# Kernel tuning notes

Measured on AMD Instinct MI355X. Metric: run time of the kernel, lower is better.

The kernel has to match this reference:

```python
import jax, jax.numpy as jnp
import numpy as np

N = 50000   # nodes
E = 800000  # edges (before self-loops)
IN = 128    # input feature dim
H = 4       # attention heads


def setup_inputs() -> dict:
    key = jax.random.key(0)
    ks = jax.random.split(key, 32)
    f = lambda k, s: (jax.random.normal(k, s, dtype=jnp.float32) * 0.1)
    inp = {
        "x": jax.random.normal(ks[0], (N, IN), dtype=jnp.float32),
        "edge_index": jax.random.randint(ks[1], (2, E), 0, N, dtype=jnp.int32),
        "edge_attr": jax.random.normal(ks[2], (E, 1), dtype=jnp.float32),
        # GATConv 1: 128 -> 8 per head, 4 heads (concat -> 32)
        "W1": f(ks[3], (IN, 32)), "as1": f(ks[4], (H, 8)), "ad1": f(ks[5], (H, 8)), "b1": jnp.zeros((32,), jnp.float32),
        # GATConv 2: 32 -> 16 per head (concat -> 64)
        "W2": f(ks[6], (32, 64)), "as2": f(ks[7], (H, 16)), "ad2": f(ks[8], (H, 16)), "b2": jnp.zeros((64,), jnp.float32),
        # GATConv 3: 64 -> 32 per head (concat -> 128)
        "W3": f(ks[9], (64, 128)), "as3": f(ks[10], (H, 32)), "ad3": f(ks[11], (H, 32)), "b3": jnp.zeros((128,), jnp.float32),
        # GATConv 4: 128 -> 64 per head (concat -> 256)
        "W4": f(ks[12], (128, 256)), "as4": f(ks[13], (H, 64)), "ad4": f(ks[14], (H, 64)), "b4": jnp.zeros((256,), jnp.float32),
        # MLP head
        "Wr": f(ks[15], (256, 32)), "br": jnp.zeros((32,), jnp.float32),
        "Wf1": f(ks[16], (32, 64)), "bf1": jnp.zeros((64,), jnp.float32),
        "Wf2": f(ks[17], (64, 1)), "bf2": jnp.zeros((1,), jnp.float32),
    }
    return inp


def _gat_layer(x, W, a_src, a_dst, bias, src, dst):
    """PyG GATConv (concat=True, negative_slope=0.2, self-loops appended upstream)."""
    heads, C = a_src.shape
    h = (x @ W).reshape(-1, heads, C)              # [N, H, C]
    alpha_s = jnp.sum(h * a_src[None], axis=-1)    # [N, H]
    alpha_d = jnp.sum(h * a_dst[None], axis=-1)    # [N, H]
    e = jax.nn.leaky_relu(alpha_s[src] + alpha_d[dst], 0.2)  # [E', H]
    # segment softmax over incoming edges of each destination node
    emax = jax.ops.segment_max(e, dst, num_segments=N)
    ee = jnp.exp(e - emax[dst])
    denom = jax.ops.segment_sum(ee, dst, num_segments=N)
    alpha = ee / denom[dst]                        # [E', H]
    msg = h[src] * alpha[:, :, None]               # [E', H, C]
    out = jax.ops.segment_sum(msg, dst, num_segments=N)  # [N, H, C]
    return out.reshape(-1, heads * C) + bias


def reference(x, edge_index, edge_attr,
              W1, as1, ad1, b1, W2, as2, ad2, b2,
              W3, as3, ad3, b3, W4, as4, ad4, b4,
              Wr, br, Wf1, bf1, Wf2, bf2):
    # edge_attr is accepted but unused, matching the original forward.
    loop = jnp.arange(N, dtype=edge_index.dtype)
    src = jnp.concatenate([edge_index[0], loop])   # add self-loops (PyG default)
    dst = jnp.concatenate([edge_index[1], loop])
    h = jax.nn.elu(_gat_layer(x, W1, as1, ad1, b1, src, dst))
    h = jax.nn.elu(_gat_layer(h, W2, as2, ad2, b2, src, dst))
    h = jax.nn.elu(_gat_layer(h, W3, as3, ad3, b3, src, dst))
    h = jax.nn.elu(_gat_layer(h, W4, as4, ad4, b4, src, dst))
    h = jax.nn.elu(h @ Wr + br)
    h = jax.nn.elu(h @ Wf1 + bf1)
    return h @ Wf2 + bf2                           # [N, 1]
```

## Files before the change

kernel.cpp:

```cpp
#include <hip/hip_runtime.h>
#include <hip/hip_fp16.h>
#include <math.h>

constexpr int NN = 50000;
constexpr int NE = 800000;
constexpr int NEP = NE + NN;
constexpr int CAP = 96;
constexpr int SCAT_B = (NEP + 255) / 256;
constexpr int PACK_B = 26;
constexpr int NT = (NN + 63) / 64;

typedef _Float16 half8_t __attribute__((ext_vector_type(8)));
typedef float    f32x4_t __attribute__((ext_vector_type(4)));

__device__ __forceinline__ float lrelu02(float x) { return x > 0.f ? x : 0.2f * x; }
__device__ __forceinline__ float eluf(float x)    { return x > 0.f ? x : (__expf(x) - 1.f); }
__device__ __forceinline__ float pick4(float4 q, int hd) {
  return (hd == 0) ? q.x : (hd == 1) ? q.y : (hd == 2) ? q.z : q.w;
}


__device__ __forceinline__ void pack_w_one(const float* __restrict__ W,
                                           __half* __restrict__ Wp,
                                           int M, int tid, int total) {
  if (tid >= total) return;
  int CT = M >> 4;
  int l = tid & 63;
  int c = (tid >> 6) % CT;
  int kc = (tid >> 6) / CT;
  int n = l & 15, q = l >> 4;
  __half* dst = Wp + (size_t)tid * 8;
  const float* src = W + (size_t)(kc * 32 + q * 8) * M + c * 16 + n;
  #pragma unroll
  for (int j = 0; j < 8; j++) dst[j] = __float2half_rn(src[j * M]);
}


template<int M, int C, int CT>
__device__ __forceinline__ void alpha_epilogue(const f32x4_t* acc,
    const float* __restrict__ a_src, const float* __restrict__ a_dst,
    int row_base, int m, float* __restrict__ as_out, float* __restrict__ ad_out) {
  float aS[CT], aD[CT];
  #pragma unroll
  for (int c = 0; c < CT; c++) { aS[c] = a_src[c * 16 + m]; aD[c] = a_dst[c * 16 + m]; }

  if constexpr (C == 8) {
    #pragma unroll
    for (int r = 0; r < 4; r++) {
      float p0 = acc[0][r] * aS[0], p1 = acc[1][r] * aS[1];
      float q0 = acc[0][r] * aD[0], q1 = acc[1][r] * aD[1];
      #pragma unroll
      for (int off = 1; off < 8; off <<= 1) {
        p0 += __shfl_xor(p0, off); p1 += __shfl_xor(p1, off);
        q0 += __shfl_xor(q0, off); q1 += __shfl_xor(q1, off);
      }
      int row = row_base + r;
      if ((m & 7) == 0 && row < NN) {
        int hb = m >> 3;
        as_out[row * 4 + hb]     = p0;
        as_out[row * 4 + 2 + hb] = p1;
        ad_out[row * 4 + hb]     = q0;
        ad_out[row * 4 + 2 + hb] = q1;
      }
    }
  } else {
    constexpr int FPH = C / 16;
    #pragma unroll
    for (int r = 0; r < 4; r++) {
      float bs[4] = {0.f, 0.f, 0.f, 0.f}, bd[4] = {0.f, 0.f, 0.f, 0.f};
      #pragma unroll
      for (int c = 0; c < CT; c++) {
        int hd = c / FPH;
        bs[hd] += acc[c][r] * aS[c];
        bd[hd] += acc[c][r] * aD[c];
      }
      #pragma unroll
      for (int off = 1; off < 16; off <<= 1)
        #pragma unroll
        for (int h = 0; h < 4; h++) {
          bs[h] += __shfl_xor(bs[h], off);
          bd[h] += __shfl_xor(bd[h], off);
        }
      int row = row_base + r;
      if (m < 4 && row < NN) {
        float vs = (m == 0) ? bs[0] : (m == 1) ? bs[1] : (m == 2) ? bs[2] : bs[3];
        float vd = (m == 0) ? bd[0] : (m == 1) ? bd[1] : (m == 2) ? bd[2] : bd[3];
        as_out[row * 4 + m] = vs;
        ad_out[row * 4 + m] = vd;
      }
    }
  }
}


__global__ __launch_bounds__(256) void front_kernel(
    const int* __restrict__ edge_src, const int* __restrict__ edge_dst,
    int* __restrict__ count, int* __restrict__ csr_src,
    const float* __restrict__ W1,
    const float* __restrict__ W2, __half* __restrict__ Wp2,
    const float* __restrict__ W3, __half* __restrict__ Wp3,
    const float* __restrict__ W4, __half* __restrict__ Wp4,
    const float* __restrict__ Wr, __half* __restrict__ Wrp,
    const float* __restrict__ Wf1, __half* __restrict__ Wf1p,
    const float* __restrict__ x, __half* __restrict__ Ch,
    const float* __restrict__ a_src, const float* __restrict__ a_dst,
    float* __restrict__ as_out, float* __restrict__ ad_out) {
  int b = blockIdx.x;
  if (b < SCAT_B) {
    int i = b * 256 + threadIdx.x;
    if (i < NEP) {
      int s, d;
      if (i < NE) { s = edge_src[i]; d = edge_dst[i]; } else { s = i - NE; d = s; }
      int pos = atomicAdd(&count[d], 1);
      if (pos < CAP) csr_src[d * CAP + pos] = s;
    }
    return;
  }
  if (b < SCAT_B + PACK_B) {
    int tid = (b - SCAT_B) * 256 + threadIdx.x;
    if (tid < 256)            pack_w_one(W2, Wp2, 64,  tid,        256);
    else if (tid < 1280)      pack_w_one(W3, Wp3, 128, tid - 256,  1024);
    else if (tid < 5376)      pack_w_one(W4, Wp4, 256, tid - 1280, 4096);
    else if (tid < 6400)      pack_w_one(Wr, Wrp, 32,  tid - 5376, 1024);
    else if (tid < 6656)      pack_w_one(Wf1, Wf1p, 64, tid - 6400, 256);
    return;
  }

  constexpr int M = 32, K = 128, CT = 2, KC = 4;
  __shared__ _Float16 Ah[64 * 40];
  __shared__ _Float16 Bs[KC * CT * 64 * 8];
  int t = threadIdx.x;
  int w = t >> 6, l = t & 63;
  int m = l & 15, q = l >> 4;
  int row0 = (b - SCAT_B - PACK_B) * 64;

  #pragma unroll
  for (int u0 = 0; u0 < 2; u0++) {
    int u = t + u0 * 256;
    int ul = u & 63;
    int uc = (u >> 6) & 1;
    int ukc = u >> 7;
    int un = ul & 15, uq = ul >> 4;
    const float* src = W1 + (size_t)(ukc * 32 + uq * 8) * M + uc * 16 + un;
    _Float16* dst = &Bs[u * 8];
    #pragma unroll
    for (int j = 0; j < 8; j++) dst[j] = (_Float16)src[j * M];
  }

  f32x4_t acc[CT];
  #pragma unroll
  for (int c = 0; c < CT; c++) acc[c] = (f32x4_t){0.f, 0.f, 0.f, 0.f};

  for (int kc = 0; kc < KC; kc++) {
    __syncthreads();
    #pragma unroll
    for (int i = 0; i < 2; i++) {
      int idx = t + 256 * i;
      int row = idx >> 3, c4 = idx & 7;
      int gr = row0 + row; if (gr >= NN) gr = NN - 1;
      float4 v = *(const float4*)(x + (size_t)gr * K + kc * 32 + c4 * 4);
      _Float16 h4[4] = {(_Float16)v.x, (_Float16)v.y, (_Float16)v.z, (_Float16)v.w};
      *(uint2*)(&Ah[row * 40 + c4 * 4]) = *(const uint2*)h4;
    }
    __syncthreads();
    half8_t a = *(const half8_t*)(&Ah[(w * 16 + m) * 40 + q * 8]);
    #pragma unroll
    for (int c = 0; c < CT; c++) {
      half8_t bf = *(const half8_t*)(&Bs[((kc * CT + c) * 64 + l) * 8]);
      acc[c] = __builtin_amdgcn_mfma_f32_16x16x32_f16(a, bf, acc[c], 0, 0, 0);
    }
  }

  #pragma unroll
  for (int r = 0; r < 4; r++) {
    int row = row0 + w * 16 + q * 4 + r;
    if (row < NN) {
      #pragma unroll
      for (int c = 0; c < CT; c++)
        Ch[(size_t)row * M + c * 16 + m] = __float2half_rn(acc[c][r]);
    }
  }
  alpha_epilogue<M, 8, CT>(acc, a_src, a_dst, row0 + w * 16 + q * 4, m, as_out, ad_out);
}


template<int M, int K, int C>
__global__ __launch_bounds__(256) void gemm_mfma_f16_kernel(const __half* __restrict__ A,
    const __half* __restrict__ Wp, __half* __restrict__ Ch,
    const float* __restrict__ a_src, const float* __restrict__ a_dst,
    float* __restrict__ as_out, float* __restrict__ ad_out) {
  constexpr int CT = M / 16;
  constexpr int KC = K / 32;
  __shared__ _Float16 Ah[64 * 40];
  int t = threadIdx.x;
  int w = t >> 6, l = t & 63;
  int m = l & 15, q = l >> 4;
  int row0 = blockIdx.x * 64;

  f32x4_t acc[CT];
  #pragma unroll
  for (int c = 0; c < CT; c++) acc[c] = (f32x4_t){0.f, 0.f, 0.f, 0.f};

  const half8_t* Bfrag = (const half8_t*)Wp;

  for (int kc = 0; kc < KC; kc++) {
    __syncthreads();
    {
      int row = t >> 2, c8 = t & 3;
      int gr = row0 + row; if (gr >= NN) gr = NN - 1;
      uint4 v = *(const uint4*)(A + (size_t)gr * K + kc * 32 + c8 * 8);
      *(uint4*)(&Ah[row * 40 + c8 * 8]) = v;
    }
    __syncthreads();
    half8_t a = *(const half8_t*)(&Ah[(w * 16 + m) * 40 + q * 8]);
    #pragma unroll
    for (int c = 0; c < CT; c++) {
      half8_t b = Bfrag[(kc * CT + c) * 64 + l];
      acc[c] = __builtin_amdgcn_mfma_f32_16x16x32_f16(a, b, acc[c], 0, 0, 0);
    }
  }

  #pragma unroll
  for (int r = 0; r < 4; r++) {
    int row = row0 + w * 16 + q * 4 + r;
    if (row < NN) {
      #pragma unroll
      for (int c = 0; c < CT; c++)
        Ch[(size_t)row * M + c * 16 + m] = __float2half_rn(acc[c][r]);
    }
  }
  alpha_epilogue<M, C, CT>(acc, a_src, a_dst, row0 + w * 16 + q * 4, m, as_out, ad_out);
}


template<int HC, int C>
__global__ __launch_bounds__(256) void agg_kernel(const __half* __restrict__ h,
    const float* __restrict__ as_v, const float* __restrict__ ad_v,
    const int* __restrict__ count, const int* __restrict__ csr_src,
    const float* __restrict__ bias, __half* __restrict__ out) {
  constexpr int V = HC / 8;
  constexpr int G = 64 / V;
  constexpr int P = 4;
  __shared__ float4 see4[4][CAP];
  __shared__ int    ssrc[4][CAP];
  int wid = threadIdx.x >> 6, lane = threadIdx.x & 63;
  int dst = blockIdx.x * 4 + wid;
  int base = dst * CAP;
  int deg = count[dst]; if (deg > CAP) deg = CAP;
  float4 ad = *(const float4*)(ad_v + dst * 4);

  float d0 = 0.f, d1 = 0.f, d2 = 0.f, d3 = 0.f;
  #pragma unroll
  for (int it = 0; it < 2; it++) {
    int j = lane + it * 64;
    if (j < deg) {
      int s = csr_src[base + j];
      float4 as = *(const float4*)(as_v + s * 4);
      float4 x = make_float4(__expf(lrelu02(as.x + ad.x)), __expf(lrelu02(as.y + ad.y)),
                             __expf(lrelu02(as.z + ad.z)), __expf(lrelu02(as.w + ad.w)));
      ssrc[wid][j] = s; see4[wid][j] = x;
      d0 += x.x; d1 += x.y; d2 += x.z; d3 += x.w;
    }
  }
  #pragma unroll
  for (int off = 32; off > 0; off >>= 1) {
    d0 += __shfl_xor(d0, off); d1 += __shfl_xor(d1, off);
    d2 += __shfl_xor(d2, off); d3 += __shfl_xor(d3, off);
  }
  float4 inv = make_float4(1.f / d0, 1.f / d1, 1.f / d2, 1.f / d3);

  int g = lane / V, v = lane % V;
  int hd = (v * 8) / C;
  float invh = pick4(inv, hd);
  int steps = (deg + G - 1) / G;
  const float4* hrows = (const float4*)h;

  float  px[P];
  float4 hv[P];
  #pragma unroll
  for (int k = 0; k < P; k++) {
    int jj = k * G + g;
    bool ok = jj < deg;
    int jc = ok ? jj : 0;
    int s = ssrc[wid][jc];
    float x = ((const float*)&see4[wid][jc])[hd];
    px[k] = ok ? x * invh : 0.f;
    hv[k] = hrows[(size_t)s * V + v];
  }

  float acc[8];
  #pragma unroll
  for (int i = 0; i < 8; i++) acc[i] = 0.f;
  int nB = (steps + P - 1) / P;
  for (int b = 1; b <= nB; b++) {
    #pragma unroll
    for (int k = 0; k < P; k++) {
      const __half2* hp = (const __half2*)&hv[k];
      float2 f0 = __half22float2(hp[0]);
      float2 f1 = __half22float2(hp[1]);
      float2 f2 = __half22float2(hp[2]);
      float2 f3 = __half22float2(hp[3]);
      float p = px[k];
      acc[0] += p * f0.x; acc[1] += p * f0.y;
      acc[2] += p * f1.x; acc[3] += p * f1.y;
      acc[4] += p * f2.x; acc[5] += p * f2.y;
      acc[6] += p * f3.x; acc[7] += p * f3.y;
      int jj = (b * P + k) * G + g;
      bool ok = jj < deg;
      int jc = ok ? jj : 0;
      int s = ssrc[wid][jc];
      float x = ((const float*)&see4[wid][jc])[hd];
      px[k] = ok ? x * invh : 0.f;
      hv[k] = hrows[(size_t)s * V + v];
    }
  }

  #pragma unroll
  for (int off = V; off < 64; off <<= 1)
    #pragma unroll
    for (int i = 0; i < 8; i++) acc[i] += __shfl_xor(acc[i], off);

  if (lane < V) {
    const float4* b4 = (const float4*)bias;
    float4 ba = b4[2 * v], bb = b4[2 * v + 1];
    _Float16 o[8];
    o[0] = (_Float16)eluf(acc[0] + ba.x); o[1] = (_Float16)eluf(acc[1] + ba.y);
    o[2] = (_Float16)eluf(acc[2] + ba.z); o[3] = (_Float16)eluf(acc[3] + ba.w);
    o[4] = (_Float16)eluf(acc[4] + bb.x); o[5] = (_Float16)eluf(acc[5] + bb.y);
    o[6] = (_Float16)eluf(acc[6] + bb.z); o[7] = (_Float16)eluf(acc[7] + bb.w);
    *(uint4*)(out + (size_t)dst * HC + v * 8) = *(const uint4*)o;
  }
}


__global__ __launch_bounds__(256) void mlp_mfma_kernel(const __half* __restrict__ h4,
    const __half* __restrict__ Wrp, const float* __restrict__ br,
    const __half* __restrict__ Wf1p, const float* __restrict__ bf1,
    const float* __restrict__ Wf2, const float* __restrict__ bf2,
    float* __restrict__ out) {
  __shared__ _Float16 rS[64 * 40];
  int t = threadIdx.x;
  int w = t >> 6, l = t & 63;
  int m = l & 15, q = l >> 4;
  int row0 = blockIdx.x * 64;
  const half8_t* Bwr  = (const half8_t*)Wrp;
  const half8_t* Bwf1 = (const half8_t*)Wf1p;

  int arow = row0 + w * 16 + m; if (arow >= NN) arow = NN - 1;
  const half8_t* Arow = (const half8_t*)(h4 + (size_t)arow * 256);
  half8_t afr[8];
  #pragma unroll
  for (int kc = 0; kc < 8; kc++) afr[kc] = Arow[kc * 4 + q];
  f32x4_t acc1[2];
  acc1[0] = (f32x4_t){0.f, 0.f, 0.f, 0.f};
  acc1[1] = (f32x4_t){0.f, 0.f, 0.f, 0.f};
  #pragma unroll
  for (int kc = 0; kc < 8; kc++) {
    acc1[0] = __builtin_amdgcn_mfma_f32_16x16x32_f16(afr[kc], Bwr[(kc * 2 + 0) * 64 + l], acc1[0], 0, 0, 0);
    acc1[1] = __builtin_amdgcn_mfma_f32_16x16x32_f16(afr[kc], Bwr[(kc * 2 + 1) * 64 + l], acc1[1], 0, 0, 0);
  }
  #pragma unroll
  for (int c = 0; c < 2; c++)
    #pragma unroll
    for (int r = 0; r < 4; r++) {
      float vv = eluf(acc1[c][r] + br[c * 16 + m]);
      rS[(w * 16 + q * 4 + r) * 40 + c * 16 + m] = (_Float16)vv;
    }
  __syncthreads();

  half8_t a2 = *(const half8_t*)(&rS[(w * 16 + m) * 40 + q * 8]);
  f32x4_t acc2[4];
  #pragma unroll
  for (int c = 0; c < 4; c++) acc2[c] = (f32x4_t){0.f, 0.f, 0.f, 0.f};
  #pragma unroll
  for (int c = 0; c < 4; c++)
    acc2[c] = __builtin_amdgcn_mfma_f32_16x16x32_f16(a2, Bwf1[c * 64 + l], acc2[c], 0, 0, 0);

  float wv[4] = {Wf2[m], Wf2[16 + m], Wf2[32 + m], Wf2[48 + m]};
  float rsum[4];
  #pragma unroll
  for (int r = 0; r < 4; r++) {
    float sr = 0.f;
    #pragma unroll
    for (int c = 0; c < 4; c++)
      sr += eluf(acc2[c][r] + bf1[c * 16 + m]) * wv[c];
    #pragma unroll
    for (int off = 1; off < 16; off <<= 1) sr += __shfl_xor(sr, off);
    rsum[r] = sr;
  }
  if (m == 0) {
    float b = bf2[0];
    #pragma unroll
    for (int r = 0; r < 4; r++) {
      int row = row0 + w * 16 + q * 4 + r;
      if (row < NN) out[row] = rsum[r] + b;
    }
  }
}


extern "C" void kernel_launch(void* const* d_in, const int* in_sizes, int n_in,
                              void* d_out, int out_size, void* d_ws, size_t ws_size,
                              hipStream_t stream) {
  const float* x   = (const float*)d_in[0];
  const int*   ei  = (const int*)d_in[1];
  const float* W1  = (const float*)d_in[3];
  const float* as1 = (const float*)d_in[4];
  const float* ad1 = (const float*)d_in[5];
  const float* b1  = (const float*)d_in[6];
  const float* W2  = (const float*)d_in[7];
  const float* as2 = (const float*)d_in[8];
  const float* ad2 = (const float*)d_in[9];
  const float* b2  = (const float*)d_in[10];
  const float* W3  = (const float*)d_in[11];
  const float* as3 = (const float*)d_in[12];
  const float* ad3 = (const float*)d_in[13];
  const float* b3  = (const float*)d_in[14];
  const float* W4  = (const float*)d_in[15];
  const float* as4 = (const float*)d_in[16];
  const float* ad4 = (const float*)d_in[17];
  const float* b4  = (const float*)d_in[18];
  const float* Wr  = (const float*)d_in[19];
  const float* br  = (const float*)d_in[20];
  const float* Wf1 = (const float*)d_in[21];
  const float* bf1 = (const float*)d_in[22];
  const float* Wf2 = (const float*)d_in[23];
  const float* bf2 = (const float*)d_in[24];
  float* out = (float*)d_out;

  char* p = (char*)d_ws;
  auto alloc = [&](size_t bytes) {
    char* q = p;
    p += (bytes + 255) & ~(size_t)255;
    return q;
  };
  int* count   = (int*)alloc((size_t)NN * 4);
  int* csr_src = (int*)alloc((size_t)NN * CAP * 4);
  __half* Hh = (__half*)alloc((size_t)NN * 256 * 2);
  __half* B2 = (__half*)alloc((size_t)NN * 128 * 2);
  __half* B3 = (__half*)alloc((size_t)NN * 256 * 2);
  float* as_buf = (float*)alloc((size_t)NN * 4 * 4);
  float* ad_buf = (float*)alloc((size_t)NN * 4 * 4);
  __half* Wp2 = (__half*)alloc((size_t)32 * 64 * 2);
  __half* Wp3 = (__half*)alloc((size_t)64 * 128 * 2);
  __half* Wp4 = (__half*)alloc((size_t)128 * 256 * 2);
  __half* Wrp = (__half*)alloc((size_t)256 * 32 * 2);
  __half* Wf1p = (__half*)alloc((size_t)32 * 64 * 2);

  const int* edge_src = ei;
  const int* edge_dst = ei + NE;

  hipMemsetAsync(count, 0, (size_t)NN * 4, stream);
  front_kernel<<<SCAT_B + PACK_B + NT, 256, 0, stream>>>(
      edge_src, edge_dst, count, csr_src,
      W1, W2, Wp2, W3, Wp3, W4, Wp4, Wr, Wrp, Wf1, Wf1p,
      x, Hh, as1, ad1, as_buf, ad_buf);

  int gb  = NT;
  int ggb = NN / 4;

  agg_kernel<32, 8><<<ggb, 256, 0, stream>>>(Hh, as_buf, ad_buf, count, csr_src, b1, B2);

  gemm_mfma_f16_kernel<64, 32, 16><<<gb, 256, 0, stream>>>(B2, Wp2, Hh, as2, ad2, as_buf, ad_buf);
  agg_kernel<64, 16><<<ggb, 256, 0, stream>>>(Hh, as_buf, ad_buf, count, csr_src, b2, B3);

  gemm_mfma_f16_kernel<128, 64, 32><<<gb, 256, 0, stream>>>(B3, Wp3, Hh, as3, ad3, as_buf, ad_buf);
  agg_kernel<128, 32><<<ggb, 256, 0, stream>>>(Hh, as_buf, ad_buf, count, csr_src, b3, B2);

  gemm_mfma_f16_kernel<256, 128, 64><<<gb, 256, 0, stream>>>(B2, Wp4, Hh, as4, ad4, as_buf, ad_buf);
  agg_kernel<256, 64><<<ggb, 256, 0, stream>>>(Hh, as_buf, ad_buf, count, csr_src, b4, B3);

  mlp_mfma_kernel<<<gb, 256, 0, stream>>>(B3, Wrp, br, Wf1p, bf1, Wf2, bf2, out);
}
```

Baseline: 398.4 us.

## Vectorize edge scatter, implicit self-loops, pre-normalize attention, peel aggregation remainder

Measured after the change: 486.5 us. 22.1% more time.

```diff
diff --git a/kernel.cpp b/kernel.cpp
--- a/kernel.cpp
+++ b/kernel.cpp
@@ -6,7 +6,7 @@
 constexpr int NE = 800000;
 constexpr int NEP = NE + NN;
 constexpr int CAP = 96;
-constexpr int SCAT_B = (NEP + 255) / 256;
+constexpr int SCAT2_B = (NE / 4 + 255) / 256;
 constexpr int PACK_B = 26;
 constexpr int NT = (NN + 63) / 64;
 
@@ -106,18 +106,25 @@
     const float* __restrict__ a_src, const float* __restrict__ a_dst,
     float* __restrict__ as_out, float* __restrict__ ad_out) {
   int b = blockIdx.x;
-  if (b < SCAT_B) {
-    int i = b * 256 + threadIdx.x;
-    if (i < NEP) {
-      int s, d;
-      if (i < NE) { s = edge_src[i]; d = edge_dst[i]; } else { s = i - NE; d = s; }
-      int pos = atomicAdd(&count[d], 1);
-      if (pos < CAP) csr_src[d * CAP + pos] = s;
-    }
-    return;
-  }
-  if (b < SCAT_B + PACK_B) {
-    int tid = (b - SCAT_B) * 256 + threadIdx.x;
+  if (b >= NT) {
+    int b2 = b - NT;
+    if (b2 < SCAT2_B) {
+      int e0 = (b2 * 256 + threadIdx.x) * 4;
+      if (e0 < NE) {
+        int4 s4 = *(const int4*)(edge_src + e0);
+        int4 d4 = *(const int4*)(edge_dst + e0);
+        int p0 = atomicAdd(&count[d4.x], 1);
+        int p1 = atomicAdd(&count[d4.y], 1);
+        int p2 = atomicAdd(&count[d4.z], 1);
+        int p3 = atomicAdd(&count[d4.w], 1);
+        if (p0 < CAP - 1) csr_src[d4.x * CAP + p0] = s4.x;
+        if (p1 < CAP - 1) csr_src[d4.y * CAP + p1] = s4.y;
+        if (p2 < CAP - 1) csr_src[d4.z * CAP + p2] = s4.z;
+        if (p3 < CAP - 1) csr_src[d4.w * CAP + p3] = s4.w;
+      }
+      return;
+    }
+    int tid = (b2 - SCAT2_B) * 256 + threadIdx.x;
     if (tid < 256)            pack_w_one(W2, Wp2, 64,  tid,        256);
     else if (tid < 1280)      pack_w_one(W3, Wp3, 128, tid - 256,  1024);
     else if (tid < 5376)      pack_w_one(W4, Wp4, 256, tid - 1280, 4096);
@@ -132,7 +139,7 @@
   int t = threadIdx.x;
   int w = t >> 6, l = t & 63;
   int m = l & 15, q = l >> 4;
-  int row0 = (b - SCAT_B - PACK_B) * 64;
+  int row0 = b * 64;
 
   #pragma unroll
   for (int u0 = 0; u0 < 2; u0++) {
@@ -246,7 +253,8 @@
   int wid = threadIdx.x >> 6, lane = threadIdx.x & 63;
   int dst = blockIdx.x * 4 + wid;
   int base = dst * CAP;
-  int deg = count[dst]; if (deg > CAP) deg = CAP;
+  int degE = count[dst]; if (degE > CAP - 1) degE = CAP - 1;
+  int deg = degE + 1;
   float4 ad = *(const float4*)(ad_v + dst * 4);
 
   float d0 = 0.f, d1 = 0.f, d2 = 0.f, d3 = 0.f;
@@ -254,7 +262,7 @@
   for (int it = 0; it < 2; it++) {
     int j = lane + it * 64;
     if (j < deg) {
-      int s = csr_src[base + j];
+      int s = (j == 0) ? dst : csr_src[base + j - 1];
       float4 as = *(const float4*)(as_v + s * 4);
       float4 x = make_float4(__expf(lrelu02(as.x + ad.x)), __expf(lrelu02(as.y + ad.y)),
                              __expf(lrelu02(as.z + ad.z)), __expf(lrelu02(as.w + ad.w)));
@@ -269,9 +277,18 @@
   }
   float4 inv = make_float4(1.f / d0, 1.f / d1, 1.f / d2, 1.f / d3);
 
+  #pragma unroll
+  for (int it = 0; it < 2; it++) {
+    int j = lane + it * 64;
+    if (j < deg) {
+      float4 xx = see4[wid][j];
+      xx.x *= inv.x; xx.y *= inv.y; xx.z *= inv.z; xx.w *= inv.w;
+      see4[wid][j] = xx;
+    }
+  }
+
   int g = lane / V, v = lane % V;
   int hd = (v * 8) / C;
-  float invh = pick4(inv, hd);
   int steps = (deg + G - 1) / G;
   const float4* hrows = (const float4*)h;
 
@@ -284,34 +301,39 @@
     int jc = ok ? jj : 0;
     int s = ssrc[wid][jc];
     float x = ((const float*)&see4[wid][jc])[hd];
-    px[k] = ok ? x * invh : 0.f;
+    px[k] = ok ? x : 0.f;
     hv[k] = hrows[(size_t)s * V + v];
   }
 
   float acc[8];
   #pragma unroll
   for (int i = 0; i < 8; i++) acc[i] = 0.f;
-  int nB = (steps + P - 1) / P;
-  for (int b = 1; b <= nB; b++) {
+
+  int nBf = steps >> 2;
+  for (int b = 1; b <= nBf; b++) {
     #pragma unroll
     for (int k = 0; k < P; k++) {
-      const __half2* hp = (const __half2*)&hv[k];
-      float2 f0 = __half22float2(hp[0]);
-      float2 f1 = __half22float2(hp[1]);
-      float2 f2 = __half22float2(hp[2]);
-      float2 f3 = __half22float2(hp[3]);
+      const _Float16* hh = (const _Float16*)&hv[k];
       float p = px[k];
-      acc[0] += p * f0.x; acc[1] += p * f0.y;
-      acc[2] += p * f1.x; acc[3] += p * f1.y;
-      acc[4] += p * f2.x; acc[5] += p * f2.y;
-      acc[6] += p * f3.x; acc[7] += p * f3.y;
+      #pragma unroll
+      for (int i = 0; i < 8; i++) acc[i] += p * (float)hh[i];
       int jj = (b * P + k) * G + g;
       bool ok = jj < deg;
       int jc = ok ? jj : 0;
       int s = ssrc[wid][jc];
       float x = ((const float*)&see4[wid][jc])[hd];
-      px[k] = ok ? x * invh : 0.f;
+      px[k] = ok ? x : 0.f;
       hv[k] = hrows[(size_t)s * V + v];
+    }
+  }
+  int rem = steps & 3;
+  #pragma unroll
+  for (int k = 0; k < P - 1; k++) {
+    if (k < rem) {
+      const _Float16* hh = (const _Float16*)&hv[k];
+      float p = px[k];
+      #pragma unroll
+      for (int i = 0; i < 8; i++) acc[i] += p * (float)hh[i];
     }
   }
 
@@ -451,7 +473,7 @@
   const int* edge_dst = ei + NE;
 
   hipMemsetAsync(count, 0, (size_t)NN * 4, stream);
-  front_kernel<<<SCAT_B + PACK_B + NT, 256, 0, stream>>>(
+  front_kernel<<<NT + SCAT2_B + PACK_B, 256, 0, stream>>>(
       edge_src, edge_dst, count, csr_src,
       W1, W2, Wp2, W3, Wp3, W4, Wp4, Wr, Wrp, Wf1, Wf1p,
       x, Hh, as1, ad1, as_buf, ad_buf);
```
